# Kernel optimization log

Hardware: AMD Instinct MI355X
Metric: run time of the kernel (lower is better)

## Reference

```python
import jax, jax.numpy as jnp
import numpy as np
from math import sqrt

B, D, H, HD, PF, K = 256, 1024, 8, 128, 2, 4
P = PF * D        # 2048, up-projected dim
HID = H * HD      # 1024
EPS = 1e-5


def _lin_w(key, out_d, in_d):
    return jax.random.normal(key, (out_d, in_d), jnp.float32) / np.sqrt(in_d)


def setup_inputs() -> dict:
    key = jax.random.key(0)
    ks = jax.random.split(key, 16)
    inp = {
        "seq": jax.random.normal(ks[0], (B, D), jnp.float32),
        "c_tm1": jax.random.normal(ks[1], (B, H, HD, HD), jnp.float32) * 0.1,
        "n_tm1": jnp.ones((B, H, HD), jnp.float32),
        "m_tm1": jnp.zeros((B, H), jnp.float32),
        # norms
        "ln_w": jnp.ones((D,), jnp.float32), "ln_b": jnp.zeros((D,), jnp.float32),
        "gn_w": jnp.ones((HID,), jnp.float32), "gn_b": jnp.zeros((HID,), jnp.float32),
        # linears (torch Linear: y = x @ W.T + b)
        "up_l_w": _lin_w(ks[2], P, D), "up_l_b": jnp.zeros((P,), jnp.float32),
        "up_r_w": _lin_w(ks[3], HID, D), "up_r_b": jnp.zeros((HID,), jnp.float32),
        "down_w": _lin_w(ks[4], D, HID), "down_b": jnp.zeros((D,), jnp.float32),
        "Wi_w": _lin_w(ks[5], H, P), "Wi_b": jnp.zeros((H,), jnp.float32),
        "Wf_w": _lin_w(ks[6], H, P), "Wf_b": jnp.zeros((H,), jnp.float32),
        "Wo_w": _lin_w(ks[7], HID, P), "Wo_b": jnp.zeros((HID,), jnp.float32),
        "Wq_w": _lin_w(ks[8], HID, P), "Wq_b": jnp.zeros((HID,), jnp.float32),
        "Wk_w": _lin_w(ks[9], HID, P), "Wk_b": jnp.zeros((HID,), jnp.float32),
        "Wv_w": _lin_w(ks[10], HID, P), "Wv_b": jnp.zeros((HID,), jnp.float32),
        # causal conv1d (1->1 channel, kernel K) and 1x1 skip conv (no bias)
        "conv_w": jax.random.normal(ks[11], (K,), jnp.float32) / np.sqrt(K),
        "conv_b": jnp.zeros((), jnp.float32),
        "skip_w": _lin_w(ks[12], HID, P),
    }
    return inp


def _layernorm(x, w, b):
    mu = jnp.mean(x, -1, keepdims=True)
    var = jnp.mean(jnp.square(x - mu), -1, keepdims=True)
    return (x - mu) * jax.lax.rsqrt(var + EPS) * w + b


def reference(seq, c_tm1, n_tm1, m_tm1, ln_w, ln_b, gn_w, gn_b,
              up_l_w, up_l_b, up_r_w, up_r_b, down_w, down_b,
              Wi_w, Wi_b, Wf_w, Wf_b, Wo_w, Wo_b,
              Wq_w, Wq_b, Wk_w, Wk_b, Wv_w, Wv_b,
              conv_w, conv_b, skip_w):
    x_n = _layernorm(seq, ln_w, ln_b)                     # [B, D]
    x_t = x_n @ up_l_w.T + up_l_b                         # [B, P]
    r_t = x_n @ up_r_w.T + up_r_b                         # [B, HID]

    # causal conv along feature axis: left-pad K-1, cross-correlate
    xp = jnp.pad(x_t, ((0, 0), (K - 1, 0)))
    x_c = sum(conv_w[j] * xp[:, j:j + P] for j in range(K)) + conv_b
    x_c = jax.nn.silu(x_c)                                # [B, P]

    q = (x_c @ Wq_w.T + Wq_b).reshape(B, H, HD)
    k = (x_c @ Wk_w.T + Wk_b).reshape(B, H, HD) / sqrt(HD)
    v = (x_t @ Wv_w.T + Wv_b).reshape(B, H, HD)
    i_t = x_c @ Wi_w.T + Wi_b                             # [B, H]
    f_t = x_c @ Wf_w.T + Wf_b                             # [B, H]
    o_t = jax.nn.sigmoid(x_t @ Wo_w.T + Wo_b)             # [B, HID]

    # stabilized exponential gating
    m_t = jnp.maximum(f_t + m_tm1, i_t)
    i_g = jnp.exp(i_t - m_t)
    f_g = jnp.exp(f_t - m_t + m_tm1)

    vk = jnp.einsum('bhd,bhp->bhdp', v, k)                # outer-product write
    c_t = f_g[:, :, None, None] * c_tm1 + i_g[:, :, None, None] * vk
    n_t = f_g[:, :, None] * n_tm1 + i_g[:, :, None] * k

    num = jnp.einsum('bhdp,bhp->bhd', c_t, q)
    den = jnp.maximum(jnp.einsum('bhd,bhd->bh', n_t, q), 1.0)
    h_t = o_t * (num / den[:, :, None]).reshape(B, HID)   # [B, HID]

    # GroupNorm(H groups) over channels
    hg = h_t.reshape(B, H, HD)
    mu = jnp.mean(hg, -1, keepdims=True)
    var = jnp.mean(jnp.square(hg - mu), -1, keepdims=True)
    hn = ((hg - mu) * jax.lax.rsqrt(var + EPS)).reshape(B, HID) * gn_w + gn_b

    out = hn + x_c @ skip_w.T                             # 1x1 skip conv
    out = out * jax.nn.silu(r_t)
    out = out @ down_w.T + down_b
    return out + seq, c_t, n_t, m_t
```

## Files before the change

kernel.cpp:

```cpp
#include <hip/hip_runtime.h>
#include <hip/hip_bf16.h>
#include <math.h>

#define B 256
#define D 1024
#define H 8
#define HD 128
#define P 2048
#define HID 1024
#define EPS 1e-5f

typedef __hip_bfloat16 bf16;
typedef short short8 __attribute__((ext_vector_type(8)));
typedef float f32x4 __attribute__((ext_vector_type(4)));

#define AS1C(p) ((const __attribute__((address_space(1))) void*)(p))
#define AS3(p)  ((__attribute__((address_space(3))) void*)(p))

__global__ __launch_bounds__(256) void zero_kernel(float* __restrict__ p) {
    const int i = blockIdx.x * 256 + threadIdx.x;
    ((float4*)p)[i] = float4{0.f, 0.f, 0.f, 0.f};
}

struct CvtSegs { const float* src[8]; bf16* dst[8]; };

__global__ __launch_bounds__(256) void convert_kernel(CvtSegs cs) {
    const int idx = blockIdx.x * 256 + threadIdx.x;
    const float* src; bf16* dst; int base;
    if      (idx <  524288) { src = cs.src[0]; dst = cs.dst[0]; base = 0; }
    else if (idx <  786432) { src = cs.src[1]; dst = cs.dst[1]; base = 524288; }
    else if (idx < 1310720) { src = cs.src[2]; dst = cs.dst[2]; base = 786432; }
    else if (idx < 1835008) { src = cs.src[3]; dst = cs.dst[3]; base = 1310720; }
    else if (idx < 2359296) { src = cs.src[4]; dst = cs.dst[4]; base = 1835008; }
    else if (idx < 2883584) { src = cs.src[5]; dst = cs.dst[5]; base = 2359296; }
    else if (idx < 3407872) { src = cs.src[6]; dst = cs.dst[6]; base = 2883584; }
    else                    { src = cs.src[7]; dst = cs.dst[7]; base = 3407872; }
    const int j = idx - base;
    const float4 v = ((const float4*)src)[j];
    union { bf16 h[4]; uint2 u; } tmp;
    tmp.h[0] = __float2bfloat16(v.x); tmp.h[1] = __float2bfloat16(v.y);
    tmp.h[2] = __float2bfloat16(v.z); tmp.h[3] = __float2bfloat16(v.w);
    *(uint2*)&dst[4 * j] = tmp.u;
}

__global__ __launch_bounds__(256) void ln_kernel(
    const float* __restrict__ seq, const float* __restrict__ w,
    const float* __restrict__ b, bf16* __restrict__ xn)
{
    const int row = blockIdx.x;
    const int tid = threadIdx.x;
    const int lane = tid & 63, wv = tid >> 6;
    const float* x = seq + (size_t)row * D;
    __shared__ float red[8];

    float vals[4];
    float s = 0.f, s2 = 0.f;
#pragma unroll
    for (int i = 0; i < 4; ++i) {
        float v = x[tid + 256 * i];
        vals[i] = v; s += v; s2 += v * v;
    }
#pragma unroll
    for (int off = 32; off; off >>= 1) {
        s  += __shfl_down(s, off, 64);
        s2 += __shfl_down(s2, off, 64);
    }
    if (lane == 0) { red[wv] = s; red[4 + wv] = s2; }
    __syncthreads();
    const float tot  = red[0] + red[1] + red[2] + red[3];
    const float tot2 = red[4] + red[5] + red[6] + red[7];
    const float mu = tot * (1.f / D);
    const float var = tot2 * (1.f / D) - mu * mu;
    const float rs = rsqrtf(var + EPS);
#pragma unroll
    for (int i = 0; i < 4; ++i) {
        const int c = tid + 256 * i;
        xn[(size_t)row * D + c] = __float2bfloat16((vals[i] - mu) * rs * w[c] + b[c]);
    }
}

struct Segs {
    const bf16* A[5];
    const bf16* W[5];
    float* O[5];
    int ostride[5];
};

__global__ __launch_bounds__(256) void gemm_bf16_sk(Segs segs, int K, int KS) {
    const int nt = blockIdx.x;
    const int seg = nt >> 4, nloc = nt & 15;
    const int m0 = blockIdx.y * 64;
    const int k0 = blockIdx.z * KS;
    const bf16* Ab = segs.A[seg];
    const bf16* Wb = segs.W[seg] + (size_t)(nloc * 64) * K;

    __shared__ bf16 As[2][64 * 32];
    __shared__ bf16 Bs[2][64 * 32];

    const int tid = threadIdx.x;
    const int srow = tid >> 2, scol = (tid & 3) * 8;
    const bf16* gA = Ab + (size_t)(m0 + srow) * K + k0 + scol;
    const bf16* gB = Wb + (size_t)srow * K + k0 + scol;

    const int lane = tid & 63, wave = tid >> 6;
    const int wm = (wave >> 1) * 32, wn = (wave & 1) * 32;
    const int fr = lane & 15, fk = (lane >> 4) * 8;
    const int aoff = (wm + fr) * 32 + fk;
    const int boff = (wn + fr) * 32 + fk;

    f32x4 acc00 = {0.f, 0.f, 0.f, 0.f};
    f32x4 acc01 = {0.f, 0.f, 0.f, 0.f};
    f32x4 acc10 = {0.f, 0.f, 0.f, 0.f};
    f32x4 acc11 = {0.f, 0.f, 0.f, 0.f};

    const int nIter = KS >> 5;

    __builtin_amdgcn_global_load_lds(AS1C(gA), AS3(&As[0][tid * 8]), 16, 0, 0);
    __builtin_amdgcn_global_load_lds(AS1C(gB), AS3(&Bs[0][tid * 8]), 16, 0, 0);

    int buf = 0;
    for (int it = 0; it < nIter; ++it) {
        __syncthreads();
        if (it + 1 < nIter) {
            const int ko = (it + 1) * 32;
            __builtin_amdgcn_global_load_lds(AS1C(gA + ko), AS3(&As[buf ^ 1][tid * 8]), 16, 0, 0);
            __builtin_amdgcn_global_load_lds(AS1C(gB + ko), AS3(&Bs[buf ^ 1][tid * 8]), 16, 0, 0);
        }
        const short8 a0 = *(const short8*)&As[buf][aoff];
        const short8 a1 = *(const short8*)&As[buf][aoff + 512];
        const short8 b0 = *(const short8*)&Bs[buf][boff];
        const short8 b1 = *(const short8*)&Bs[buf][boff + 512];
        acc00 = __builtin_amdgcn_mfma_f32_16x16x32_bf16(a0, b0, acc00, 0, 0, 0);
        acc01 = __builtin_amdgcn_mfma_f32_16x16x32_bf16(a0, b1, acc01, 0, 0, 0);
        acc10 = __builtin_amdgcn_mfma_f32_16x16x32_bf16(a1, b0, acc10, 0, 0, 0);
        acc11 = __builtin_amdgcn_mfma_f32_16x16x32_bf16(a1, b1, acc11, 0, 0, 0);
        buf ^= 1;
    }

    float* Ob = segs.O[seg] + nloc * 64 + wn;
    const int ost = segs.ostride[seg];
    const int r0 = m0 + wm + (lane >> 4) * 4;
    const int c0 = lane & 15;
#pragma unroll
    for (int r = 0; r < 4; ++r) {
        atomicAdd(&Ob[(size_t)(r0 + r) * ost + c0],           acc00[r]);
        atomicAdd(&Ob[(size_t)(r0 + r) * ost + 16 + c0],      acc01[r]);
        atomicAdd(&Ob[(size_t)(r0 + r + 16) * ost + c0],      acc10[r]);
        atomicAdd(&Ob[(size_t)(r0 + r + 16) * ost + 16 + c0], acc11[r]);
    }
}

__global__ __launch_bounds__(256) void conv_kernel(
    const float* __restrict__ xtacc, const float* __restrict__ ulb,
    const float* __restrict__ cw, const float* __restrict__ cb,
    bf16* __restrict__ xt_bf, float* __restrict__ xc, bf16* __restrict__ xc_bf)
{
    const int idx = blockIdx.x * 256 + threadIdx.x;
    const int b = idx >> 11, i = idx & 2047;
    const float* row = xtacc + (size_t)b * P;
    const float x0 = row[i] + ulb[i];
    xt_bf[idx] = __float2bfloat16(x0);
    float acc = cb[0] + cw[3] * x0;
    if (i >= 1) acc = fmaf(cw[2], row[i - 1] + ulb[i - 1], acc);
    if (i >= 2) acc = fmaf(cw[1], row[i - 2] + ulb[i - 2], acc);
    if (i >= 3) acc = fmaf(cw[0], row[i - 3] + ulb[i - 3], acc);
    const float sv = acc / (1.f + expf(-acc));
    xc[idx] = sv;
    xc_bf[idx] = __float2bfloat16(sv);
}

__global__ __launch_bounds__(256) void if_kernel(
    const float* __restrict__ xc,
    const float* __restrict__ Wi, const float* __restrict__ Wib,
    const float* __restrict__ Wf, const float* __restrict__ Wfb,
    float* __restrict__ it, float* __restrict__ ft)
{
    const int blk = blockIdx.x;
    const int b = blk >> 3, h = blk & 7;
    const int tid = threadIdx.x;
    const int lane = tid & 63, wv = tid >> 6;
    const float* x = xc + (size_t)b * P;
    const float* wi = Wi + (size_t)h * P;
    const float* wf = Wf + (size_t)h * P;
    float pi = 0.f, pf = 0.f;
    for (int p = tid; p < P; p += 256) {
        const float xv = x[p];
        pi = fmaf(xv, wi[p], pi);
        pf = fmaf(xv, wf[p], pf);
    }
    __shared__ float red[8];
#pragma unroll
    for (int off = 32; off; off >>= 1) {
        pi += __shfl_down(pi, off, 64);
        pf += __shfl_down(pf, off, 64);
    }
    if (lane == 0) { red[wv] = pi; red[4 + wv] = pf; }
    __syncthreads();
    if (tid == 0) {
        it[blk] = red[0] + red[1] + red[2] + red[3] + Wib[h];
        ft[blk] = red[4] + red[5] + red[6] + red[7] + Wfb[h];
    }
}

__global__ __launch_bounds__(256) void gate_kernel(
    const float* __restrict__ c_tm1, const float* __restrict__ n_tm1,
    const float* __restrict__ m_tm1, const float* __restrict__ it_a,
    const float* __restrict__ ft_a,
    const float* __restrict__ qacc, const float* __restrict__ kacc,
    const float* __restrict__ vacc, const float* __restrict__ oacc,
    const float* __restrict__ sacc, const float* __restrict__ racc,
    const float* __restrict__ qb, const float* __restrict__ kb,
    const float* __restrict__ vb, const float* __restrict__ ob,
    const float* __restrict__ rb,
    const float* __restrict__ gn_w, const float* __restrict__ gn_b,
    float* __restrict__ c_out, float* __restrict__ n_out,
    float* __restrict__ m_out, bf16* __restrict__ y)
{
    const int blk = blockIdx.x;
    const int b = blk >> 3, h = blk & 7;
    const int tid = threadIdx.x;
    const int lane = tid & 63, wv = tid >> 6;
    const float kscale = 0.08838834764831845f;

    __shared__ float sk_[128], sq_[128], sv_[128], snum[128];
    __shared__ float red[8];

    const float it = it_a[blk], ft = ft_a[blk], mp = m_tm1[blk];
    const float mt = fmaxf(ft + mp, it);
    const float ig = expf(it - mt);
    const float fg = expf(ft - mt + mp);
    if (tid == 0) m_out[blk] = mt;

    const int col0 = h * HD;
    const int hid_off = b * HID + col0;
    float den_p = 0.f;
    if (tid < 128) {
        const int col = col0 + tid;
        const float kd = (kacc[hid_off + tid] + kb[col]) * kscale;
        const float qd = qacc[hid_off + tid] + qb[col];
        sk_[tid] = kd; sq_[tid] = qd;
        sv_[tid] = vacc[hid_off + tid] + vb[col];
        const float nn = fg * n_tm1[(size_t)blk * HD + tid] + ig * kd;
        n_out[(size_t)blk * HD + tid] = nn;
        den_p = nn * qd;
    }
    __syncthreads();
#pragma unroll
    for (int off = 32; off; off >>= 1) den_p += __shfl_down(den_p, off, 64);
    if (lane == 0) red[wv] = den_p;
    __syncthreads();
    const float den = fmaxf(red[0] + red[1] + red[2] + red[3], 1.0f);

    const float k0 = sk_[2 * lane], k1 = sk_[2 * lane + 1];
    const float q0 = sq_[2 * lane], q1 = sq_[2 * lane + 1];
    const size_t cbase = (size_t)blk * (HD * HD);
#pragma unroll 4
    for (int r = 0; r < 32; ++r) {
        const int d = r * 4 + wv;
        const float2 c2 = *(const float2*)(c_tm1 + cbase + d * HD + 2 * lane);
        const float a = ig * sv_[d];
        const float c0v = fmaf(fg, c2.x, a * k0);
        const float c1v = fmaf(fg, c2.y, a * k1);
        float2 st; st.x = c0v; st.y = c1v;
        *(float2*)(c_out + cbase + d * HD + 2 * lane) = st;
        float psum = c0v * q0 + c1v * q1;
#pragma unroll
        for (int off = 32; off; off >>= 1) psum += __shfl_down(psum, off, 64);
        if (lane == 0) snum[d] = psum;
    }
    __syncthreads();

    float hval = 0.f, s1 = 0.f, s2 = 0.f;
    if (tid < 128) {
        const int col = col0 + tid;
        const float ot = 1.f / (1.f + expf(-(oacc[hid_off + tid] + ob[col])));
        hval = ot * snum[tid] / den;
        s1 = hval; s2 = hval * hval;
    }
#pragma unroll
    for (int off = 32; off; off >>= 1) {
        s1 += __shfl_down(s1, off, 64);
        s2 += __shfl_down(s2, off, 64);
    }
    if (lane == 0) { red[wv] = s1; red[4 + wv] = s2; }
    __syncthreads();
    const float mu = (red[0] + red[1] + red[2] + red[3]) * (1.f / HD);
    const float ms = (red[4] + red[5] + red[6] + red[7]) * (1.f / HD);
    const float var = ms - mu * mu;
    if (tid < 128) {
        const int col = col0 + tid;
        const float hn = (hval - mu) * rsqrtf(var + EPS) * gn_w[col] + gn_b[col];
        const float sr = racc[hid_off + tid] + rb[col];
        const float silu_r = sr / (1.f + expf(-sr));
        y[hid_off + tid] = __float2bfloat16((hn + sacc[hid_off + tid]) * silu_r);
    }
}

__global__ __launch_bounds__(256) void e3_kernel(
    const float* __restrict__ dacc, const float* __restrict__ db,
    const float* __restrict__ seq, float* __restrict__ out)
{
    const int i = blockIdx.x * 256 + threadIdx.x;
    const float4 d = ((const float4*)dacc)[i];
    const float4 s = ((const float4*)seq)[i];
    const float4 bb = ((const float4*)db)[i & 255];
    float4 o;
    o.x = d.x + s.x + bb.x; o.y = d.y + s.y + bb.y;
    o.z = d.z + s.z + bb.z; o.w = d.w + s.w + bb.w;
    ((float4*)out)[i] = o;
}

extern "C" void kernel_launch(void* const* d_in, const int* in_sizes, int n_in,
                              void* d_out, int out_size, void* d_ws, size_t ws_size,
                              hipStream_t stream) {
    const float* seq    = (const float*)d_in[0];
    const float* c_tm1  = (const float*)d_in[1];
    const float* n_tm1  = (const float*)d_in[2];
    const float* m_tm1  = (const float*)d_in[3];
    const float* ln_w   = (const float*)d_in[4];
    const float* ln_b   = (const float*)d_in[5];
    const float* gn_w   = (const float*)d_in[6];
    const float* gn_b   = (const float*)d_in[7];
    const float* up_l_w = (const float*)d_in[8];
    const float* up_l_b = (const float*)d_in[9];
    const float* up_r_w = (const float*)d_in[10];
    const float* up_r_b = (const float*)d_in[11];
    const float* down_w = (const float*)d_in[12];
    const float* down_b = (const float*)d_in[13];
    const float* Wi_w   = (const float*)d_in[14];
    const float* Wi_b   = (const float*)d_in[15];
    const float* Wf_w   = (const float*)d_in[16];
    const float* Wf_b   = (const float*)d_in[17];
    const float* Wo_w   = (const float*)d_in[18];
    const float* Wo_b   = (const float*)d_in[19];
    const float* Wq_w   = (const float*)d_in[20];
    const float* Wq_b   = (const float*)d_in[21];
    const float* Wk_w   = (const float*)d_in[22];
    const float* Wk_b   = (const float*)d_in[23];
    const float* Wv_w   = (const float*)d_in[24];
    const float* Wv_b   = (const float*)d_in[25];
    const float* conv_w = (const float*)d_in[26];
    const float* conv_b = (const float*)d_in[27];
    const float* skip_w = (const float*)d_in[28];

    float* ws = (float*)d_ws;
    float* xtacc = ws;
    float* racc  = ws + 524288;
    float* qacc  = ws + 786432;
    float* kacc  = ws + 1048576;
    float* vacc  = ws + 1310720;
    float* oacc  = ws + 1572864;
    float* sacc  = ws + 1835008;
    float* dacc  = ws + 2097152;
    float* itb   = ws + 2359296;
    float* ftb   = ws + 2361344;
    bf16* yb_bf   = (bf16*)(ws + 2363392);
    bf16* down_bf = (bf16*)(ws + 2494464);

    float* out0  = (float*)d_out;
    float* c_out = out0 + 262144;
    float* n_out = out0 + 33816576;
    float* m_out = out0 + 34078720;

    bf16* wbuf   = (bf16*)c_out;
    bf16* upl_bf = wbuf;
    bf16* upr_bf = wbuf + 2097152;
    bf16* wq_bf  = wbuf + 3145728;
    bf16* wk_bf  = wbuf + 5242880;
    bf16* wv_bf  = wbuf + 7340032;
    bf16* wo_bf  = wbuf + 9437184;
    bf16* wsk_bf = wbuf + 11534336;
    bf16* xn_bf  = wbuf + 13631488;
    bf16* xt_bf  = wbuf + 13893632;
    bf16* xc_bf  = wbuf + 14417920;
    float* xc_f  = (float*)(wbuf + 14942208);

    zero_kernel<<<2304, 256, 0, stream>>>(ws);

    CvtSegs cv;
    cv.src[0] = up_l_w; cv.dst[0] = upl_bf;
    cv.src[1] = up_r_w; cv.dst[1] = upr_bf;
    cv.src[2] = Wq_w;   cv.dst[2] = wq_bf;
    cv.src[3] = Wk_w;   cv.dst[3] = wk_bf;
    cv.src[4] = Wv_w;   cv.dst[4] = wv_bf;
    cv.src[5] = Wo_w;   cv.dst[5] = wo_bf;
    cv.src[6] = skip_w; cv.dst[6] = wsk_bf;
    cv.src[7] = down_w; cv.dst[7] = down_bf;
    convert_kernel<<<14336, 256, 0, stream>>>(cv);

    ln_kernel<<<B, 256, 0, stream>>>(seq, ln_w, ln_b, xn_bf);

    Segs g1{};
    g1.A[0] = xn_bf; g1.W[0] = upl_bf;               g1.O[0] = xtacc;        g1.ostride[0] = P;
    g1.A[1] = xn_bf; g1.W[1] = upl_bf + 1024 * 1024; g1.O[1] = xtacc + 1024; g1.ostride[1] = P;
    g1.A[2] = xn_bf; g1.W[2] = upr_bf;               g1.O[2] = racc;         g1.ostride[2] = HID;
    gemm_bf16_sk<<<dim3(48, 4, 4), 256, 0, stream>>>(g1, 1024, 256);

    conv_kernel<<<(B * P) / 256, 256, 0, stream>>>(
        xtacc, up_l_b, conv_w, conv_b, xt_bf, xc_f, xc_bf);

    Segs g2{};
    g2.A[0] = xc_bf; g2.W[0] = wq_bf;  g2.O[0] = qacc; g2.ostride[0] = HID;
    g2.A[1] = xc_bf; g2.W[1] = wk_bf;  g2.O[1] = kacc; g2.ostride[1] = HID;
    g2.A[2] = xt_bf; g2.W[2] = wv_bf;  g2.O[2] = vacc; g2.ostride[2] = HID;
    g2.A[3] = xt_bf; g2.W[3] = wo_bf;  g2.O[3] = oacc; g2.ostride[3] = HID;
    g2.A[4] = xc_bf; g2.W[4] = wsk_bf; g2.O[4] = sacc; g2.ostride[4] = HID;
    gemm_bf16_sk<<<dim3(80, 4, 2), 256, 0, stream>>>(g2, 2048, 1024);

    if_kernel<<<B * H, 256, 0, stream>>>(xc_f, Wi_w, Wi_b, Wf_w, Wf_b, itb, ftb);

    gate_kernel<<<B * H, 256, 0, stream>>>(
        c_tm1, n_tm1, m_tm1, itb, ftb,
        qacc, kacc, vacc, oacc, sacc, racc,
        Wq_b, Wk_b, Wv_b, Wo_b, up_r_b, gn_w, gn_b,
        c_out, n_out, m_out, yb_bf);

    Segs g3{};
    g3.A[0] = yb_bf; g3.W[0] = down_bf; g3.O[0] = dacc; g3.ostride[0] = HID;
    gemm_bf16_sk<<<dim3(16, 4, 4), 256, 0, stream>>>(g3, 1024, 256);

    e3_kernel<<<256, 256, 0, stream>>>(dacc, down_b, seq, out0);
}
```

Measured before the change: 394.4 us.

## Add 128x128 split-K GEMM tile and vectorize gate kernel cell-state update

```diff
diff --git a/kernel.cpp b/kernel.cpp
--- a/kernel.cpp
+++ b/kernel.cpp
@@ -148,6 +148,74 @@
         atomicAdd(&Ob[(size_t)(r0 + r + 16) * ost + c0],      acc10[r]);
         atomicAdd(&Ob[(size_t)(r0 + r + 16) * ost + 16 + c0], acc11[r]);
     }
+}
+
+__global__ __launch_bounds__(256) void gemm128_sk(Segs segs, int K, int KS) {
+    const int nt = blockIdx.x;
+    const int seg = nt >> 3, nloc = nt & 7;
+    const int m0 = blockIdx.y * 128;
+    const int k0 = blockIdx.z * KS;
+    const bf16* Ab = segs.A[seg];
+    const bf16* Wb = segs.W[seg] + (size_t)(nloc * 128) * K;
+
+    __shared__ bf16 As[2][128 * 32];
+    __shared__ bf16 Bs[2][128 * 32];
+
+    const int tid = threadIdx.x;
+    const int srow = tid >> 2, scol = (tid & 3) * 8;
+    const bf16* gA = Ab + (size_t)(m0 + srow) * K + k0 + scol;
+    const bf16* gB = Wb + (size_t)srow * K + k0 + scol;
+    const size_t rowK64 = (size_t)64 * K;
+
+    const int lane = tid & 63, wave = tid >> 6;
+    const int wm = (wave >> 1) * 64, wn = (wave & 1) * 64;
+    const int fr = lane & 15, fk = (lane >> 4) * 8;
+    const int aoff = (wm + fr) * 32 + fk;
+    const int boff = (wn + fr) * 32 + fk;
+
+    f32x4 acc[4][4] = {};
+
+    const int nIter = KS >> 5;
+
+    __builtin_amdgcn_global_load_lds(AS1C(gA),          AS3(&As[0][tid * 8]),        16, 0, 0);
+    __builtin_amdgcn_global_load_lds(AS1C(gA + rowK64), AS3(&As[0][2048 + tid * 8]), 16, 0, 0);
+    __builtin_amdgcn_global_load_lds(AS1C(gB),          AS3(&Bs[0][tid * 8]),        16, 0, 0);
+    __builtin_amdgcn_global_load_lds(AS1C(gB + rowK64), AS3(&Bs[0][2048 + tid * 8]), 16, 0, 0);
+
+    int buf = 0;
+    for (int it = 0; it < nIter; ++it) {
+        __syncthreads();
+        if (it + 1 < nIter) {
+            const int ko = (it + 1) * 32;
+            __builtin_amdgcn_global_load_lds(AS1C(gA + ko),          AS3(&As[buf ^ 1][tid * 8]),        16, 0, 0);
+            __builtin_amdgcn_global_load_lds(AS1C(gA + ko + rowK64), AS3(&As[buf ^ 1][2048 + tid * 8]), 16, 0, 0);
+            __builtin_amdgcn_global_load_lds(AS1C(gB + ko),          AS3(&Bs[buf ^ 1][tid * 8]),        16, 0, 0);
+            __builtin_amdgcn_global_load_lds(AS1C(gB + ko + rowK64), AS3(&Bs[buf ^ 1][2048 + tid * 8]), 16, 0, 0);
+        }
+        short8 a[4], bb[4];
+#pragma unroll
+        for (int i = 0; i < 4; ++i) a[i]  = *(const short8*)&As[buf][aoff + i * 512];
+#pragma unroll
+        for (int j = 0; j < 4; ++j) bb[j] = *(const short8*)&Bs[buf][boff + j * 512];
+#pragma unroll
+        for (int i = 0; i < 4; ++i)
+#pragma unroll
+            for (int j = 0; j < 4; ++j)
+                acc[i][j] = __builtin_amdgcn_mfma_f32_16x16x32_bf16(a[i], bb[j], acc[i][j], 0, 0, 0);
+        buf ^= 1;
+    }
+
+    float* Ob = segs.O[seg] + nloc * 128 + wn;
+    const int ost = segs.ostride[seg];
+    const int r0 = m0 + wm + (lane >> 4) * 4;
+    const int c0 = lane & 15;
+#pragma unroll
+    for (int i = 0; i < 4; ++i)
+#pragma unroll
+        for (int j = 0; j < 4; ++j)
+#pragma unroll
+            for (int r = 0; r < 4; ++r)
+                atomicAdd(&Ob[(size_t)(r0 + i * 16 + r) * ost + j * 16 + c0], acc[i][j][r]);
 }
 
 __global__ __launch_bounds__(256) void conv_kernel(
@@ -222,7 +290,10 @@
     const int lane = tid & 63, wv = tid >> 6;
     const float kscale = 0.08838834764831845f;
 
-    __shared__ float sk_[128], sq_[128], sv_[128], snum[128];
+    __shared__ __align__(16) float sk_[128];
+    __shared__ __align__(16) float sq_[128];
+    __shared__ __align__(16) float sv_[128];
+    __shared__ __align__(16) float snum[128];
     __shared__ float red[8];
 
     const float it = it_a[blk], ft = ft_a[blk], mp = m_tm1[blk];
@@ -251,22 +322,36 @@
     __syncthreads();
     const float den = fmaxf(red[0] + red[1] + red[2] + red[3], 1.0f);
 
-    const float k0 = sk_[2 * lane], k1 = sk_[2 * lane + 1];
-    const float q0 = sq_[2 * lane], q1 = sq_[2 * lane + 1];
+    const int g4 = tid >> 2;
+    const int l4 = tid & 3;
+    const int pbase = l4 * 4;
     const size_t cbase = (size_t)blk * (HD * HD);
-#pragma unroll 4
-    for (int r = 0; r < 32; ++r) {
-        const int d = r * 4 + wv;
-        const float2 c2 = *(const float2*)(c_tm1 + cbase + d * HD + 2 * lane);
+#pragma unroll
+    for (int rr = 0; rr < 2; ++rr) {
+        const int d = g4 + rr * 64;
         const float a = ig * sv_[d];
-        const float c0v = fmaf(fg, c2.x, a * k0);
-        const float c1v = fmaf(fg, c2.y, a * k1);
-        float2 st; st.x = c0v; st.y = c1v;
-        *(float2*)(c_out + cbase + d * HD + 2 * lane) = st;
-        float psum = c0v * q0 + c1v * q1;
-#pragma unroll
-        for (int off = 32; off; off >>= 1) psum += __shfl_down(psum, off, 64);
-        if (lane == 0) snum[d] = psum;
+        const float* crow = c_tm1 + cbase + (size_t)d * HD;
+        float* orow = c_out + cbase + (size_t)d * HD;
+        float ps = 0.f;
+#pragma unroll
+        for (int j = 0; j < 8; ++j) {
+            const int p = j * 16 + pbase;
+            float4 c4 = *(const float4*)(crow + p);
+            const float4 k4 = *(const float4*)&sk_[p];
+            const float4 q4 = *(const float4*)&sq_[p];
+            c4.x = fmaf(fg, c4.x, a * k4.x);
+            c4.y = fmaf(fg, c4.y, a * k4.y);
+            c4.z = fmaf(fg, c4.z, a * k4.z);
+            c4.w = fmaf(fg, c4.w, a * k4.w);
+            *(float4*)(orow + p) = c4;
+            ps = fmaf(c4.x, q4.x, ps);
+            ps = fmaf(c4.y, q4.y, ps);
+            ps = fmaf(c4.z, q4.z, ps);
+            ps = fmaf(c4.w, q4.w, ps);
+        }
+        ps += __shfl_xor(ps, 1, 64);
+        ps += __shfl_xor(ps, 2, 64);
+        if (l4 == 0) snum[d] = ps;
     }
     __syncthreads();
 
@@ -394,7 +479,7 @@
     g1.A[0] = xn_bf; g1.W[0] = upl_bf;               g1.O[0] = xtacc;        g1.ostride[0] = P;
     g1.A[1] = xn_bf; g1.W[1] = upl_bf + 1024 * 1024; g1.O[1] = xtacc + 1024; g1.ostride[1] = P;
     g1.A[2] = xn_bf; g1.W[2] = upr_bf;               g1.O[2] = racc;         g1.ostride[2] = HID;
-    gemm_bf16_sk<<<dim3(48, 4, 4), 256, 0, stream>>>(g1, 1024, 256);
+    gemm128_sk<<<dim3(24, 2, 8), 256, 0, stream>>>(g1, 1024, 128);
 
     conv_kernel<<<(B * P) / 256, 256, 0, stream>>>(
         xtacc, up_l_b, conv_w, conv_b, xt_bf, xc_f, xc_bf);
@@ -405,7 +490,7 @@
     g2.A[2] = xt_bf; g2.W[2] = wv_bf;  g2.O[2] = vacc; g2.ostride[2] = HID;
     g2.A[3] = xt_bf; g2.W[3] = wo_bf;  g2.O[3] = oacc; g2.ostride[3] = HID;
     g2.A[4] = xc_bf; g2.W[4] = wsk_bf; g2.O[4] = sacc; g2.ostride[4] = HID;
-    gemm_bf16_sk<<<dim3(80, 4, 2), 256, 0, stream>>>(g2, 2048, 1024);
+    gemm128_sk<<<dim3(40, 2, 8), 256, 0, stream>>>(g2, 2048, 256);
 
     if_kernel<<<B * H, 256, 0, stream>>>(xc_f, Wi_w, Wi_b, Wf_w, Wf_b, itb, ftb);
 
```

After: 436.4 us. 10.7% more time.
